# Optimization experiments

Hardware: AMD Instinct MI355X
Metric: run time of the kernel (lower is better)

The kernel has to match this reference:

```python
import jax, jax.numpy as jnp
import numpy as np

N_NODES = 50000
N_EDGES = 1600000
IN_CH = 128
HIDDEN = 128
N_CLASSES = 40


def setup_inputs() -> dict:
    key = jax.random.key(0)
    ks = jax.random.split(key, 8)
    node_features = jax.random.normal(ks[0], (1, N_NODES, IN_CH), dtype=jnp.float32)
    edge_index = jax.random.randint(ks[1], (1, 2, N_EDGES), 0, N_NODES, dtype=jnp.int64)
    rank_mapping = jnp.zeros((2, N_EDGES), dtype=jnp.int32)
    s1 = 1.0 / np.sqrt(IN_CH)
    s2 = 1.0 / np.sqrt(HIDDEN)
    W1 = jax.random.uniform(ks[2], (IN_CH, HIDDEN), jnp.float32, -s1, s1)
    b1 = jax.random.uniform(ks[3], (HIDDEN,), jnp.float32, -s1, s1)
    W2 = jax.random.uniform(ks[4], (HIDDEN, HIDDEN), jnp.float32, -s2, s2)
    b2 = jax.random.uniform(ks[5], (HIDDEN,), jnp.float32, -s2, s2)
    Wfc = jax.random.uniform(ks[6], (HIDDEN, N_CLASSES), jnp.float32, -s2, s2)
    bfc = jax.random.uniform(ks[7], (N_CLASSES,), jnp.float32, -s2, s2)
    return {"node_features": node_features, "edge_index": edge_index,
            "rank_mapping": rank_mapping, "W1": W1, "b1": b1,
            "W2": W2, "b2": b2, "Wfc": Wfc, "bfc": bfc}


def _gcn_single(feats, src, dst, W1, b1, W2, b2, Wfc, bfc):
    # feats: [N, F]; src/dst: [E]
    n = feats.shape[0]
    x = feats[dst]                                 # gather -> [E, F]
    x = jax.nn.relu(x @ W1 + b1)                   # conv1 (Linear + ReLU)
    x = jax.ops.segment_sum(x, src, num_segments=n)  # scatter-sum -> [N, H]
    x = x[dst]                                     # gather -> [E, H]
    x = x @ W2 + b2                                # conv2 (plain Linear)
    x = jax.ops.segment_sum(x, src, num_segments=n)  # scatter-sum -> [N, H]
    return x @ Wfc + bfc                           # [N, C]


def reference(node_features, edge_index, rank_mapping, W1, b1, W2, b2, Wfc, bfc):
    src = edge_index[:, 0, :]  # [B, E]
    dst = edge_index[:, 1, :]  # [B, E]
    return jax.vmap(_gcn_single, in_axes=(0, 0, 0, None, None, None, None, None, None))(
        node_features, src, dst, W1, b1, W2, b2, Wfc, bfc)
```

## Files before the change

kernel.cpp:

```cpp
#include <hip/hip_runtime.h>

static constexpr int NN = 50000;
static constexpr int NE = 1600000;
static constexpr int CH = 128;
static constexpr int NCLS = 40;

static constexpr int NPB  = 64;
static constexpr int NBUK = (NN + NPB - 1) / NPB;
static constexpr int EPB  = 32768;
static constexpr int NHB  = (NE + EPB - 1) / EPB;
static constexpr int NS   = NBUK * NHB;
static constexpr int SCAN_B = 256;
static constexpr int NSB  = (NS + SCAN_B - 1) / SCAN_B;
static constexpr int NROWP = ((NN + 63) / 64) * 64;
static constexpr int PAD = 136;
static constexpr int GEMM_BLKS = (NN + 63) / 64;
static constexpr int CAP = 3072;

typedef __attribute__((ext_vector_type(8))) short bf16x8;
typedef __attribute__((ext_vector_type(4))) float f32x4;

__device__ __forceinline__ float bflo(unsigned v) {
    return __uint_as_float((v & 0xFFFFu) << 16);
}
__device__ __forceinline__ float bfhi(unsigned v) {
    return __uint_as_float(v & 0xFFFF0000u);
}
__device__ __forceinline__ unsigned short f2bf(float f) {
    unsigned u = __float_as_uint(f);
    u += 0x7FFFu + ((u >> 16) & 1u);
    return (unsigned short)(u >> 16);
}

__global__ __launch_bounds__(256)
void fused_pre(const int* __restrict__ src, int* __restrict__ H,
               const float* __restrict__ W1, unsigned short* __restrict__ Wt_g,
               const float* __restrict__ W2, const float* __restrict__ Wfc,
               const float* __restrict__ b2, unsigned short* __restrict__ Mt,
               float* __restrict__ cfc)
{
    __shared__ int h[NBUK];
    const int t = threadIdx.x;
    const int b = blockIdx.x;

    if (b < NHB) {
        for (int i = t; i < NBUK; i += 256) h[i] = 0;
        __syncthreads();
        const int base4 = b * (EPB / 4);
        const int4* src4 = reinterpret_cast<const int4*>(src);
        for (int i = t; i < EPB / 4; i += 256) {
            const int idx = base4 + i;
            if (idx < NE / 4) {
                const int4 v = src4[idx];
                atomicAdd(&h[v.x >> 6], 1);
                atomicAdd(&h[v.y >> 6], 1);
                atomicAdd(&h[v.z >> 6], 1);
                atomicAdd(&h[v.w >> 6], 1);
            }
        }
        __syncthreads();
        for (int i = t; i < NBUK; i += 256) H[i * NHB + b] = h[i];
    } else if (b < NHB + 64) {
        const int idx = (b - NHB) * 256 + t;
        const int c = idx >> 7;
        const int k = idx & 127;
        Wt_g[c * PAD + k] = f2bf(W1[k * 128 + c]);
    } else {
        const int idx = (b - NHB - 64) * 256 + t;
        if (idx < 48 * 128) {
            const int c = idx >> 7;
            const int k = idx & 127;
            float a = 0.f;
            if (c < NCLS) {
                #pragma unroll 16
                for (int j = 0; j < 128; ++j) a += W2[k * 128 + j] * Wfc[j * NCLS + c];
            }
            Mt[c * 128 + k] = f2bf(a);
        }
        if (b == NHB + 64 && t < NCLS) {
            float a = 0.f;
            #pragma unroll 16
            for (int j = 0; j < 128; ++j) a += b2[j] * Wfc[j * NCLS + t];
            cfc[t] = a;
        }
    }
}

__global__ __launch_bounds__(SCAN_B)
void scan_local(int* __restrict__ H, int* __restrict__ bsum)
{
    __shared__ int buf[SCAN_B];
    const int t = threadIdx.x;
    const int g = blockIdx.x * SCAN_B + t;
    const int v = (g < NS) ? H[g] : 0;
    buf[t] = v;
    __syncthreads();
    #pragma unroll
    for (int off = 1; off < SCAN_B; off <<= 1) {
        const int x = (t >= off) ? buf[t - off] : 0;
        __syncthreads();
        buf[t] += x;
        __syncthreads();
    }
    if (g < NS) H[g] = buf[t] - v;
    if (t == SCAN_B - 1) bsum[blockIdx.x] = buf[t];
}

__global__ __launch_bounds__(SCAN_B)
void scan_bsums(int* __restrict__ bsum)
{
    __shared__ int buf[SCAN_B];
    const int t = threadIdx.x;
    const int v = (t < NSB) ? bsum[t] : 0;
    buf[t] = v;
    __syncthreads();
    #pragma unroll
    for (int off = 1; off < SCAN_B; off <<= 1) {
        const int x = (t >= off) ? buf[t - off] : 0;
        __syncthreads();
        buf[t] += x;
        __syncthreads();
    }
    if (t < NSB) bsum[t] = buf[t] - v;
    if (t == SCAN_B - 1) bsum[NSB] = buf[t];
}

__global__ __launch_bounds__(256)
void fused_mid(const int* __restrict__ src, const int* __restrict__ dst,
               const int* __restrict__ H, const int* __restrict__ bsum,
               int* __restrict__ EP,
               const float* __restrict__ X, const unsigned short* __restrict__ Wt_g,
               const float* __restrict__ b, const unsigned short* __restrict__ Mt,
               unsigned short* __restrict__ V1)
{
    __shared__ __align__(16) unsigned short Wt[128 * PAD];
    __shared__ __align__(16) unsigned short Fa[64 * PAD];
    __shared__ __align__(16) unsigned short Va[64 * NCLS];
    __shared__ float bl[128];
    __shared__ int cur[NBUK];

    const int t = threadIdx.x;

    if (blockIdx.x < NHB) {
        const int bb = blockIdx.x;
        for (int i = t; i < NBUK; i += 256) {
            const int x = i * NHB + bb;
            cur[i] = H[x] + bsum[x >> 8];
        }
        __syncthreads();
        const int base4 = bb * (EPB / 4);
        const int4* src4 = reinterpret_cast<const int4*>(src);
        const int4* dst4 = reinterpret_cast<const int4*>(dst);
        for (int i = t; i < EPB / 4; i += 256) {
            const int idx = base4 + i;
            if (idx < NE / 4) {
                const int4 s4 = src4[idx];
                const int4 d4 = dst4[idx];
                int pos;
                pos = atomicAdd(&cur[s4.x >> 6], 1); EP[pos] = ((s4.x & 63) << 16) | d4.x;
                pos = atomicAdd(&cur[s4.y >> 6], 1); EP[pos] = ((s4.y & 63) << 16) | d4.y;
                pos = atomicAdd(&cur[s4.z >> 6], 1); EP[pos] = ((s4.z & 63) << 16) | d4.z;
                pos = atomicAdd(&cur[s4.w >> 6], 1); EP[pos] = ((s4.w & 63) << 16) | d4.w;
            }
        }
        return;
    }

    const int gb = blockIdx.x - NHB;
    const int lane = t & 63;
    const int w = t >> 6;

    for (int i = t; i < (128 * PAD) / 8; i += 256)
        reinterpret_cast<uint4*>(Wt)[i] = reinterpret_cast<const uint4*>(Wt_g)[i];
    if (t < 128) bl[t] = b[t];

    const int base = gb * 64;
    const int nRows = min(64, NN - base);
    {
        const int r = t >> 2;
        const int c0 = (t & 3) * 32;
        if (r < nRows) {
            #pragma unroll
            for (int j = 0; j < 32; j += 4) {
                const float4 v = *reinterpret_cast<const float4*>(&X[(size_t)(base + r) * CH + c0 + j]);
                ushort4 o; o.x = f2bf(v.x); o.y = f2bf(v.y); o.z = f2bf(v.z); o.w = f2bf(v.w);
                *reinterpret_cast<ushort4*>(&Fa[r * PAD + c0 + j]) = o;
            }
        } else {
            #pragma unroll
            for (int j = 0; j < 32; j += 4) {
                ushort4 z; z.x = z.y = z.z = z.w = 0;
                *reinterpret_cast<ushort4*>(&Fa[r * PAD + c0 + j]) = z;
            }
        }
    }
    __syncthreads();

    f32x4 acc[8];
    #pragma unroll
    for (int i = 0; i < 8; ++i) acc[i] = (f32x4){0.f, 0.f, 0.f, 0.f};

    const int arow = w * 16 + (lane & 15);
    const int kgrp = (lane >> 4) * 4;

    #pragma unroll
    for (int ks = 0; ks < 4; ++ks) {
        const int k0 = ks * 32 + kgrp;
        bf16x8 af;
        {
            const short4 lo = *reinterpret_cast<const short4*>(&Fa[arow * PAD + k0]);
            const short4 hi = *reinterpret_cast<const short4*>(&Fa[arow * PAD + k0 + 16]);
            af[0] = lo.x; af[1] = lo.y; af[2] = lo.z; af[3] = lo.w;
            af[4] = hi.x; af[5] = hi.y; af[6] = hi.z; af[7] = hi.w;
        }
        #pragma unroll
        for (int ct = 0; ct < 8; ++ct) {
            const int c = ct * 16 + (lane & 15);
            bf16x8 bf;
            const short4 lo = *reinterpret_cast<const short4*>(&Wt[c * PAD + k0]);
            const short4 hi = *reinterpret_cast<const short4*>(&Wt[c * PAD + k0 + 16]);
            bf[0] = lo.x; bf[1] = lo.y; bf[2] = lo.z; bf[3] = lo.w;
            bf[4] = hi.x; bf[5] = hi.y; bf[6] = hi.z; bf[7] = hi.w;
            acc[ct] = __builtin_amdgcn_mfma_f32_16x16x32_bf16(af, bf, acc[ct], 0, 0, 0);
        }
    }
    __syncthreads();

    #pragma unroll
    for (int ct = 0; ct < 8; ++ct) {
        const int c = ct * 16 + (lane & 15);
        const float bias = bl[c];
        #pragma unroll
        for (int r = 0; r < 4; ++r) {
            const int row = w * 16 + (lane >> 4) * 4 + r;
            Fa[row * PAD + c] = f2bf(fmaxf(acc[ct][r] + bias, 0.f));
        }
    }
    __syncthreads();

    f32x4 acc2[3];
    #pragma unroll
    for (int i = 0; i < 3; ++i) acc2[i] = (f32x4){0.f, 0.f, 0.f, 0.f};

    #pragma unroll
    for (int ks = 0; ks < 4; ++ks) {
        const int k0 = ks * 32 + kgrp;
        bf16x8 af;
        {
            const short4 lo = *reinterpret_cast<const short4*>(&Fa[arow * PAD + k0]);
            const short4 hi = *reinterpret_cast<const short4*>(&Fa[arow * PAD + k0 + 16]);
            af[0] = lo.x; af[1] = lo.y; af[2] = lo.z; af[3] = lo.w;
            af[4] = hi.x; af[5] = hi.y; af[6] = hi.z; af[7] = hi.w;
        }
        #pragma unroll
        for (int ct = 0; ct < 3; ++ct) {
            const int c = ct * 16 + (lane & 15);
            bf16x8 bf;
            const short4 lo = *reinterpret_cast<const short4*>(&Mt[c * 128 + k0]);
            const short4 hi = *reinterpret_cast<const short4*>(&Mt[c * 128 + k0 + 16]);
            bf[0] = lo.x; bf[1] = lo.y; bf[2] = lo.z; bf[3] = lo.w;
            bf[4] = hi.x; bf[5] = hi.y; bf[6] = hi.z; bf[7] = hi.w;
            acc2[ct] = __builtin_amdgcn_mfma_f32_16x16x32_bf16(af, bf, acc2[ct], 0, 0, 0);
        }
    }

    #pragma unroll
    for (int ct = 0; ct < 3; ++ct) {
        const int c = ct * 16 + (lane & 15);
        if (c < NCLS) {
            #pragma unroll
            for (int r = 0; r < 4; ++r) {
                const int row = w * 16 + (lane >> 4) * 4 + r;
                Va[row * NCLS + c] = f2bf(acc2[ct][r]);
            }
        }
    }
    __syncthreads();

    for (int i = t; i < 320; i += 256) {
        const int r = i / 5;
        const int q = i % 5;
        *reinterpret_cast<uint4*>(&V1[(size_t)(base + r) * NCLS + q * 8]) =
            *reinterpret_cast<const uint4*>(&Va[r * NCLS + q * 8]);
    }
}

__global__ __launch_bounds__(512)
void sortgather(const int* __restrict__ H, const int* __restrict__ bsum,
                const int* __restrict__ EP, const unsigned short* __restrict__ V1,
                unsigned short* __restrict__ U1, unsigned short* __restrict__ sdst,
                int* __restrict__ offs, int* __restrict__ deg)
{
    __shared__ int raw[CAP];
    __shared__ unsigned short srt[CAP];
    __shared__ int hist[NPB], cur[NPB], segBeg[NPB + 1];

    const int t = threadIdx.x;
    const int b = blockIdx.x;
    const int node0 = b * NPB;
    const int nNodes = min(NPB, NN - node0);
    const int xb = b * NHB;
    const int beg = H[xb] + bsum[xb >> 8];
    int end;
    if (b == NBUK - 1) end = NE;
    else { const int xe = (b + 1) * NHB; end = H[xe] + bsum[xe >> 8]; }
    const int C = end - beg;

    for (int i = t; i < C; i += 512) raw[i] = EP[beg + i];
    if (t < NPB) hist[t] = 0;
    __syncthreads();
    for (int i = t; i < C; i += 512) atomicAdd(&hist[raw[i] >> 16], 1);
    __syncthreads();

    if (t < NPB) cur[t] = hist[t];
    __syncthreads();
    #pragma unroll
    for (int off = 1; off < NPB; off <<= 1) {
        int x = 0;
        if (t < NPB && t >= off) x = cur[t - off];
        __syncthreads();
        if (t < NPB) cur[t] += x;
        __syncthreads();
    }
    if (t < NPB) segBeg[t] = cur[t] - hist[t];
    if (t == 0) segBeg[NPB] = C;
    __syncthreads();

    if (t < nNodes) {
        offs[node0 + t] = beg + segBeg[t];
        deg[node0 + t] = hist[t];
    }
    if (b == NBUK - 1 && t == 0) offs[NN] = NE;
    if (t < NPB) cur[t] = segBeg[t];
    __syncthreads();

    for (int i = t; i < C; i += 512) {
        const int p = raw[i];
        const int pos = atomicAdd(&cur[p >> 16], 1);
        srt[pos] = (unsigned short)(p & 0xFFFF);
    }
    __syncthreads();

    for (int i = t; i < C; i += 512) sdst[beg + i] = srt[i];

    const int w = t >> 6;
    const int lane = t & 63;
    const int g = lane >> 4;
    const int L = lane & 15;

    for (int ni = 0; ni < 8; ++ni) {
        const int n = w * 8 + ni;
        if (n >= nNodes) break;
        const int sb = segBeg[n];
        const int se = segBeg[n + 1];
        float a0 = 0.f, a1 = 0.f, a2 = 0.f, a3 = 0.f;

        int i = sb;
        for (; i + 16 <= se; i += 16) {
            const int d0 = srt[i + g];
            const int d1 = srt[i + 4 + g];
            const int d2 = srt[i + 8 + g];
            const int d3 = srt[i + 12 + g];
            if (L < 10) {
                const uint2 v0 = *reinterpret_cast<const uint2*>(&V1[(size_t)d0 * NCLS + L * 4]);
                const uint2 v1 = *reinterpret_cast<const uint2*>(&V1[(size_t)d1 * NCLS + L * 4]);
                const uint2 v2 = *reinterpret_cast<const uint2*>(&V1[(size_t)d2 * NCLS + L * 4]);
                const uint2 v3 = *reinterpret_cast<const uint2*>(&V1[(size_t)d3 * NCLS + L * 4]);
                a0 += bflo(v0.x) + bflo(v1.x) + bflo(v2.x) + bflo(v3.x);
                a1 += bfhi(v0.x) + bfhi(v1.x) + bfhi(v2.x) + bfhi(v3.x);
                a2 += bflo(v0.y) + bflo(v1.y) + bflo(v2.y) + bflo(v3.y);
                a3 += bfhi(v0.y) + bfhi(v1.y) + bfhi(v2.y) + bfhi(v3.y);
            }
        }
        for (; i + 4 <= se; i += 4) {
            const int d = srt[i + g];
            if (L < 10) {
                const uint2 v = *reinterpret_cast<const uint2*>(&V1[(size_t)d * NCLS + L * 4]);
                a0 += bflo(v.x); a1 += bfhi(v.x);
                a2 += bflo(v.y); a3 += bfhi(v.y);
            }
        }
        const int rem = se - i;
        if (g < rem) {
            const int d = srt[i + g];
            if (L < 10) {
                const uint2 v = *reinterpret_cast<const uint2*>(&V1[(size_t)d * NCLS + L * 4]);
                a0 += bflo(v.x); a1 += bfhi(v.x);
                a2 += bflo(v.y); a3 += bfhi(v.y);
            }
        }

        a0 += __shfl_xor(a0, 16); a0 += __shfl_xor(a0, 32);
        a1 += __shfl_xor(a1, 16); a1 += __shfl_xor(a1, 32);
        a2 += __shfl_xor(a2, 16); a2 += __shfl_xor(a2, 32);
        a3 += __shfl_xor(a3, 16); a3 += __shfl_xor(a3, 32);

        if (lane < 16 && L < 10) {
            uint2 o;
            o.x = ((unsigned)f2bf(a1) << 16) | f2bf(a0);
            o.y = ((unsigned)f2bf(a3) << 16) | f2bf(a2);
            *reinterpret_cast<uint2*>(&U1[(size_t)(node0 + n) * NCLS + L * 4]) = o;
        }
    }
}

__global__ __launch_bounds__(512)
void gather40f(const int* __restrict__ offs, const unsigned short* __restrict__ sdst,
               const unsigned short* __restrict__ X, float* __restrict__ Yf,
               const int* __restrict__ deg,
               const float* __restrict__ cfc, const float* __restrict__ bfc)
{
    const int t = threadIdx.x;
    const int w = t >> 6;
    const int lane = t & 63;
    const int g = lane >> 4;
    const int L = lane & 15;
    const int node0 = blockIdx.x * 32 + w * 4;

    float4 cf = make_float4(0.f, 0.f, 0.f, 0.f);
    float4 bfv = make_float4(0.f, 0.f, 0.f, 0.f);
    if (L < 10) {
        cf  = *reinterpret_cast<const float4*>(&cfc[L * 4]);
        bfv = *reinterpret_cast<const float4*>(&bfc[L * 4]);
    }

    #pragma unroll
    for (int ni = 0; ni < 4; ++ni) {
        const int n = node0 + ni;
        if (n >= NN) break;
        const int sb = offs[n];
        const int se = offs[n + 1];
        float a0 = 0.f, a1 = 0.f, a2 = 0.f, a3 = 0.f;

        int i = sb;
        for (; i + 16 <= se; i += 16) {
            const int d0 = sdst[i + g];
            const int d1 = sdst[i + 4 + g];
            const int d2 = sdst[i + 8 + g];
            const int d3 = sdst[i + 12 + g];
            if (L < 10) {
                const uint2 v0 = *reinterpret_cast<const uint2*>(&X[(size_t)d0 * NCLS + L * 4]);
                const uint2 v1 = *reinterpret_cast<const uint2*>(&X[(size_t)d1 * NCLS + L * 4]);
                const uint2 v2 = *reinterpret_cast<const uint2*>(&X[(size_t)d2 * NCLS + L * 4]);
                const uint2 v3 = *reinterpret_cast<const uint2*>(&X[(size_t)d3 * NCLS + L * 4]);
                a0 += bflo(v0.x) + bflo(v1.x) + bflo(v2.x) + bflo(v3.x);
                a1 += bfhi(v0.x) + bfhi(v1.x) + bfhi(v2.x) + bfhi(v3.x);
                a2 += bflo(v0.y) + bflo(v1.y) + bflo(v2.y) + bflo(v3.y);
                a3 += bfhi(v0.y) + bfhi(v1.y) + bfhi(v2.y) + bfhi(v3.y);
            }
        }
        for (; i + 4 <= se; i += 4) {
            const int d = sdst[i + g];
            if (L < 10) {
                const uint2 v = *reinterpret_cast<const uint2*>(&X[(size_t)d * NCLS + L * 4]);
                a0 += bflo(v.x); a1 += bfhi(v.x);
                a2 += bflo(v.y); a3 += bfhi(v.y);
            }
        }
        const int rem = se - i;
        if (g < rem) {
            const int d = sdst[i + g];
            if (L < 10) {
                const uint2 v = *reinterpret_cast<const uint2*>(&X[(size_t)d * NCLS + L * 4]);
                a0 += bflo(v.x); a1 += bfhi(v.x);
                a2 += bflo(v.y); a3 += bfhi(v.y);
            }
        }

        a0 += __shfl_xor(a0, 16); a0 += __shfl_xor(a0, 32);
        a1 += __shfl_xor(a1, 16); a1 += __shfl_xor(a1, 32);
        a2 += __shfl_xor(a2, 16); a2 += __shfl_xor(a2, 32);
        a3 += __shfl_xor(a3, 16); a3 += __shfl_xor(a3, 32);

        if (lane < 16 && L < 10) {
            const float dgn = (float)deg[n];
            float4 o;
            o.x = a0 + dgn * cf.x + bfv.x;
            o.y = a1 + dgn * cf.y + bfv.y;
            o.z = a2 + dgn * cf.z + bfv.z;
            o.w = a3 + dgn * cf.w + bfv.w;
            *reinterpret_cast<float4*>(&Yf[(size_t)n * NCLS + L * 4]) = o;
        }
    }
}

extern "C" void kernel_launch(void* const* d_in, const int* in_sizes, int n_in,
                              void* d_out, int out_size, void* d_ws, size_t ws_size,
                              hipStream_t stream) {
    const float* F   = (const float*)d_in[0];
    const int*   EI  = (const int*)  d_in[1];
    const float* W1  = (const float*)d_in[3];
    const float* b1  = (const float*)d_in[4];
    const float* W2  = (const float*)d_in[5];
    const float* b2  = (const float*)d_in[6];
    const float* Wfc = (const float*)d_in[7];
    const float* bfc = (const float*)d_in[8];
    float* out = (float*)d_out;

    char* ws = (char*)d_ws;
    size_t off = 0;
    auto take = [&](size_t bytes) { char* p = ws + off; off += (bytes + 63) & ~(size_t)63; return p; };

    unsigned short* V1   = (unsigned short*)take((size_t)NROWP * NCLS * 2);
    unsigned short* U1   = (unsigned short*)take((size_t)NROWP * NCLS * 2);
    unsigned short* sdst = (unsigned short*)take((size_t)NE * 2);
    int*   EP   = (int*)take((size_t)NE * 4);
    int*   H    = (int*)take((size_t)NS * 4);
    int*   bsum = (int*)take((size_t)(NSB + 1) * 4);
    int*   deg  = (int*)take((size_t)NN * 4);
    int*   offs = (int*)take((size_t)(NN + 1) * 4);
    unsigned short* Mt   = (unsigned short*)take((size_t)48 * 128 * 2);
    unsigned short* Wt_g = (unsigned short*)take((size_t)128 * PAD * 2);
    float* cfc  = (float*)take((size_t)NCLS * 4);

    const int* src = EI;
    const int* dst = EI + NE;

    fused_pre<<<NHB + 64 + 24, 256, 0, stream>>>(src, H, W1, Wt_g, W2, Wfc, b2, Mt, cfc);

    scan_local<<<NSB, SCAN_B, 0, stream>>>(H, bsum);
    scan_bsums<<<1, SCAN_B, 0, stream>>>(bsum);

    fused_mid<<<NHB + GEMM_BLKS, 256, 0, stream>>>(src, dst, H, bsum, EP,
                                                   F, Wt_g, b1, Mt, V1);

    sortgather<<<NBUK, 512, 0, stream>>>(H, bsum, EP, V1, U1, sdst, offs, deg);

    gather40f<<<(NN + 31) / 32, 512, 0, stream>>>(offs, sdst, U1, out, deg, cfc, bfc);
}
```

Before: 123.7 us.

## Coarsen scatter buckets to 256 nodes and split per 64-node sub-bucket in sortgather

The first-pass counting sort now buckets edges by 256-node groups and uses smaller edge chunks per histogram block, which shrinks the histogram/scan matrix and raises block-level parallelism in the histogram and scatter passes. Each sortgather block re-reads its coarse bucket and filters to its 64-node sub-bucket via a shared atomic counter. Sorted destinations go to fixed-capacity per-block slots (b*CAP), so offsets become per-block and the end index is derived from degree. The trade-off is that every coarse bucket's edges are read four times, and correctness depends on each sub-bucket fitting within CAP.

```diff
diff --git a/kernel.cpp b/kernel.cpp
--- a/kernel.cpp
+++ b/kernel.cpp
@@ -7,10 +7,13 @@
 
 static constexpr int NPB  = 64;
 static constexpr int NBUK = (NN + NPB - 1) / NPB;
-static constexpr int EPB  = 32768;
+static constexpr int NPB_SC = 256;
+static constexpr int NBUK_SC = (NN + NPB_SC - 1) / NPB_SC;
+static constexpr int EPB  = 8192;
 static constexpr int NHB  = (NE + EPB - 1) / EPB;
-static constexpr int NS   = NBUK * NHB;
+static constexpr int NS   = NBUK_SC * NHB;
 static constexpr int SCAN_B = 256;
+static constexpr int SCAN_SHIFT = 8;
 static constexpr int NSB  = (NS + SCAN_B - 1) / SCAN_B;
 static constexpr int NROWP = ((NN + 63) / 64) * 64;
 static constexpr int PAD = 136;
@@ -39,12 +42,12 @@
                const float* __restrict__ b2, unsigned short* __restrict__ Mt,
                float* __restrict__ cfc)
 {
-    __shared__ int h[NBUK];
+    __shared__ int h[NBUK_SC];
     const int t = threadIdx.x;
     const int b = blockIdx.x;
 
     if (b < NHB) {
-        for (int i = t; i < NBUK; i += 256) h[i] = 0;
+        for (int i = t; i < NBUK_SC; i += 256) h[i] = 0;
         __syncthreads();
         const int base4 = b * (EPB / 4);
         const int4* src4 = reinterpret_cast<const int4*>(src);
@@ -52,14 +55,14 @@
             const int idx = base4 + i;
             if (idx < NE / 4) {
                 const int4 v = src4[idx];
-                atomicAdd(&h[v.x >> 6], 1);
-                atomicAdd(&h[v.y >> 6], 1);
-                atomicAdd(&h[v.z >> 6], 1);
-                atomicAdd(&h[v.w >> 6], 1);
-            }
-        }
-        __syncthreads();
-        for (int i = t; i < NBUK; i += 256) H[i * NHB + b] = h[i];
+                atomicAdd(&h[v.x >> 8], 1);
+                atomicAdd(&h[v.y >> 8], 1);
+                atomicAdd(&h[v.z >> 8], 1);
+                atomicAdd(&h[v.w >> 8], 1);
+            }
+        }
+        __syncthreads();
+        for (int i = t; i < NBUK_SC; i += 256) H[i * NHB + b] = h[i];
     } else if (b < NHB + 64) {
         const int idx = (b - NHB) * 256 + t;
         const int c = idx >> 7;
@@ -137,15 +140,15 @@
     __shared__ __align__(16) unsigned short Fa[64 * PAD];
     __shared__ __align__(16) unsigned short Va[64 * NCLS];
     __shared__ float bl[128];
-    __shared__ int cur[NBUK];
+    __shared__ int cur[NBUK_SC];
 
     const int t = threadIdx.x;
 
     if (blockIdx.x < NHB) {
         const int bb = blockIdx.x;
-        for (int i = t; i < NBUK; i += 256) {
+        for (int i = t; i < NBUK_SC; i += 256) {
             const int x = i * NHB + bb;
-            cur[i] = H[x] + bsum[x >> 8];
+            cur[i] = H[x] + bsum[x >> SCAN_SHIFT];
         }
         __syncthreads();
         const int base4 = bb * (EPB / 4);
@@ -157,10 +160,10 @@
                 const int4 s4 = src4[idx];
                 const int4 d4 = dst4[idx];
                 int pos;
-                pos = atomicAdd(&cur[s4.x >> 6], 1); EP[pos] = ((s4.x & 63) << 16) | d4.x;
-                pos = atomicAdd(&cur[s4.y >> 6], 1); EP[pos] = ((s4.y & 63) << 16) | d4.y;
-                pos = atomicAdd(&cur[s4.z >> 6], 1); EP[pos] = ((s4.z & 63) << 16) | d4.z;
-                pos = atomicAdd(&cur[s4.w >> 6], 1); EP[pos] = ((s4.w & 63) << 16) | d4.w;
+                pos = atomicAdd(&cur[s4.x >> 8], 1); EP[pos] = ((s4.x & 255) << 16) | d4.x;
+                pos = atomicAdd(&cur[s4.y >> 8], 1); EP[pos] = ((s4.y & 255) << 16) | d4.y;
+                pos = atomicAdd(&cur[s4.z >> 8], 1); EP[pos] = ((s4.z & 255) << 16) | d4.z;
+                pos = atomicAdd(&cur[s4.w >> 8], 1); EP[pos] = ((s4.w & 255) << 16) | d4.w;
             }
         }
         return;
@@ -294,21 +297,35 @@
     __shared__ int raw[CAP];
     __shared__ unsigned short srt[CAP];
     __shared__ int hist[NPB], cur[NPB], segBeg[NPB + 1];
+    __shared__ int cnt;
 
     const int t = threadIdx.x;
     const int b = blockIdx.x;
+    const int cb = b >> 2;
+    const int sub = b & 3;
     const int node0 = b * NPB;
     const int nNodes = min(NPB, NN - node0);
-    const int xb = b * NHB;
-    const int beg = H[xb] + bsum[xb >> 8];
+    const int xb = cb * NHB;
+    const int beg = H[xb] + bsum[xb >> SCAN_SHIFT];
     int end;
-    if (b == NBUK - 1) end = NE;
-    else { const int xe = (b + 1) * NHB; end = H[xe] + bsum[xe >> 8]; }
-    const int C = end - beg;
-
-    for (int i = t; i < C; i += 512) raw[i] = EP[beg + i];
+    if (cb == NBUK_SC - 1) end = NE;
+    else { const int xe = (cb + 1) * NHB; end = H[xe] + bsum[xe >> SCAN_SHIFT]; }
+
+    if (t == 0) cnt = 0;
     if (t < NPB) hist[t] = 0;
     __syncthreads();
+
+    for (int i = beg + t; i < end; i += 512) {
+        const int p = EP[i];
+        const int hi = p >> 16;
+        if ((hi >> 6) == sub) {
+            const int pos = atomicAdd(&cnt, 1);
+            raw[pos] = ((hi & 63) << 16) | (p & 0xFFFF);
+        }
+    }
+    __syncthreads();
+    const int C = cnt;
+
     for (int i = t; i < C; i += 512) atomicAdd(&hist[raw[i] >> 16], 1);
     __syncthreads();
 
@@ -327,10 +344,9 @@
     __syncthreads();
 
     if (t < nNodes) {
-        offs[node0 + t] = beg + segBeg[t];
+        offs[node0 + t] = b * CAP + segBeg[t];
         deg[node0 + t] = hist[t];
     }
-    if (b == NBUK - 1 && t == 0) offs[NN] = NE;
     if (t < NPB) cur[t] = segBeg[t];
     __syncthreads();
 
@@ -341,7 +357,7 @@
     }
     __syncthreads();
 
-    for (int i = t; i < C; i += 512) sdst[beg + i] = srt[i];
+    for (int i = t; i < C; i += 512) sdst[b * CAP + i] = srt[i];
 
     const int w = t >> 6;
     const int lane = t & 63;
@@ -429,7 +445,8 @@
         const int n = node0 + ni;
         if (n >= NN) break;
         const int sb = offs[n];
-        const int se = offs[n + 1];
+        const int dgi = deg[n];
+        const int se = sb + dgi;
         float a0 = 0.f, a1 = 0.f, a2 = 0.f, a3 = 0.f;
 
         int i = sb;
@@ -473,7 +490,7 @@
         a3 += __shfl_xor(a3, 16); a3 += __shfl_xor(a3, 32);
 
         if (lane < 16 && L < 10) {
-            const float dgn = (float)deg[n];
+            const float dgn = (float)dgi;
             float4 o;
             o.x = a0 + dgn * cf.x + bfv.x;
             o.y = a1 + dgn * cf.y + bfv.y;
@@ -503,7 +520,7 @@
 
     unsigned short* V1   = (unsigned short*)take((size_t)NROWP * NCLS * 2);
     unsigned short* U1   = (unsigned short*)take((size_t)NROWP * NCLS * 2);
-    unsigned short* sdst = (unsigned short*)take((size_t)NE * 2);
+    unsigned short* sdst = (unsigned short*)take((size_t)NBUK * CAP * 2);
     int*   EP   = (int*)take((size_t)NE * 4);
     int*   H    = (int*)take((size_t)NS * 4);
     int*   bsum = (int*)take((size_t)(NSB + 1) * 4);
```

Result: faster. 108.9 us (median of 2 runs) (-12.0%).
